# Performance work log

Measured on AMD Instinct MI355X. Metric: run time of the kernel, lower is better.

The kernel has to match this reference:

```python
import jax, jax.numpy as jnp
import numpy as np

T, N, F_IN, DZ = 4, 2048, 128, 128
HF = 256   # FEM output dim
H = 256    # EDM hidden dim
E1, E2 = 256, 64  # EAM dims


def _l2norm(x, axis):
    n = jnp.sqrt(jnp.sum(x * x, axis=axis, keepdims=True))
    return x / jnp.maximum(n, 1e-12)


def setup_inputs() -> dict:
    key = jax.random.key(0)
    ks = jax.random.split(key, 20)

    def lin(k, fi, fo):
        return (jax.random.normal(k, (fi, fo), jnp.float32) / np.float32(np.sqrt(fi)))

    sup = jax.random.uniform(ks[0], (T, N, N), jnp.float32)
    sup = sup / jnp.sum(sup, axis=2, keepdims=True)       # row-normalized GNN supports
    align = jax.random.uniform(ks[1], (T, N, N), jnp.float32)
    align = align / jnp.sum(align, axis=2, keepdims=True)  # row-normalized align matrices
    feat = jax.random.normal(ks[2], (T + 1, N, F_IN), jnp.float32)
    noise = jax.random.normal(ks[3], (T, N, DZ), jnp.float32)
    G_IN = HF + DZ   # 384
    EIN = H + HF     # 512
    return {
        "sup": sup, "feat": feat, "noise": noise, "align": align,
        "lambd": jnp.float32(0.4),
        "W_fem": lin(ks[4], F_IN, HF), "b_fem": jnp.zeros((HF,), jnp.float32),
        "W_gnn": lin(ks[5], G_IN, H), "b_gnn": jnp.zeros((H,), jnp.float32),
        "Wg_x": lin(ks[6], H, 2 * H), "Wg_h": lin(ks[7], H, 2 * H), "bg": jnp.zeros((2 * H,), jnp.float32),
        "Wc_x": lin(ks[8], H, H), "Wc_h": lin(ks[9], H, H), "bc": jnp.zeros((H,), jnp.float32),
        "W_att": lin(ks[10], HF, H), "b_att": jnp.zeros((H,), jnp.float32),
        "W_emb1": lin(ks[11], EIN, E1), "b_emb1": jnp.zeros((E1,), jnp.float32),
        "W_emb2": lin(ks[12], E1, E2), "b_emb2": jnp.zeros((E2,), jnp.float32),
        "W_scal1": lin(ks[13], EIN, E1), "b_scal1": jnp.zeros((E1,), jnp.float32),
        "W_scal2": lin(ks[14], E1, E2), "b_scal2": jnp.zeros((E2,), jnp.float32),
    }


def reference(sup, feat, noise, align, lambd,
              W_fem, b_fem, W_gnn, b_gnn,
              Wg_x, Wg_h, bg, Wc_x, Wc_h, bc,
              W_att, b_att,
              W_emb1, b_emb1, W_emb2, b_emb2,
              W_scal1, b_scal1, W_scal2, b_scal2):
    # --- FEM: shared linear + relu over all T+1 snapshots ---
    fem = jax.nn.relu(jnp.einsum('tnf,fh->tnh', feat, W_fem) + b_fem)  # [T+1,N,HF]
    t_win = sup.shape[0]
    edm_in = jnp.concatenate([fem[:t_win], noise], axis=2)             # [T,N,HF+DZ]

    # --- GNN (no time recurrence -> batched over T): relu((sup@x)W), row L2-norm ---
    agg = jnp.einsum('tnm,tmf->tnf', sup, edm_in)
    g = _l2norm(jax.nn.relu(jnp.einsum('tnf,fh->tnh', agg, W_gnn) + b_gnn), axis=2)

    # attention feature maps for the attentive node-aligning unit
    fm = jnp.einsum('tnf,fh->tnh', fem, W_att) + b_att                 # [T+1,N,H]
    h0 = jnp.zeros((sup.shape[1], W_gnn.shape[1]), dtype=feat.dtype)

    def step(h, x):
        gt, al, fsrc, fdst = x
        # IGRU cell
        gates = jax.nn.sigmoid(gt @ Wg_x + h @ Wg_h + bg)
        r, u = jnp.split(gates, 2, axis=1)
        c = jnp.tanh(gt @ Wc_x + (r * h) @ Wc_h + bc)
        rnn = (1.0 - u) * h + u * c
        # attentive node aligning: mix given align matrix with feature attention
        att = jax.nn.softmax(fdst @ fsrc.T, axis=1)                    # [N,N]
        sup_al = lambd * al + (1.0 - lambd) * att
        h_new = sup_al @ rnn
        return h_new, None

    h_last, _ = jax.lax.scan(step, h0, (g, align, fm[:t_win], fm[1:]))

    # --- EAM (pred_flag=True): tanh embedding head + sigmoid scaling head ---
    emb_cat = jnp.concatenate([h_last, fem[t_win]], axis=1)            # [N, H+HF]
    emb = jnp.tanh(jnp.tanh(emb_cat @ W_emb1 + b_emb1) @ W_emb2 + b_emb2)
    emb = _l2norm(emb, axis=0)                                         # F.normalize(dim=0)
    scal_o = jax.nn.sigmoid(jax.nn.sigmoid(emb_cat @ W_scal1 + b_scal1) @ W_scal2 + b_scal2)
    scal = scal_o @ scal_o.T                                           # [N,N]
    # pairwise-distance decoder: adj[i,j] = 1 + tanh(-||e_i - e_j||^2 * scal[i,j])
    sq = jnp.sum(emb * emb, axis=1)
    dist = -(sq[:, None] + sq[None, :] - 2.0 * (emb @ emb.T))
    return 1.0 + jnp.tanh(dist * scal)
```

## Files before the change

kernel.cpp:

```cpp
#include <hip/hip_runtime.h>
#include <math.h>


#define T_WIN 4
#define NN 2048
#define F_IN 128
#define HF 256
#define HH 256
#define DZ 128
#define G_IN 384
#define EIN 512
#define E1D 256
#define E2D 64

typedef _Float16 f16;
typedef _Float16 f16x8 __attribute__((ext_vector_type(8)));
typedef _Float16 f16x4 __attribute__((ext_vector_type(4)));
typedef float f32x4 __attribute__((ext_vector_type(4)));

__device__ __forceinline__ float wave_sum(float v) {
#pragma unroll
  for (int o = 32; o > 0; o >>= 1) v += __shfl_down(v, o);
  return v;
}
__device__ __forceinline__ float wave_max(float v) {
#pragma unroll
  for (int o = 32; o > 0; o >>= 1) v = fmaxf(v, __shfl_down(v, o));
  return v;
}

__device__ __forceinline__ void gld_lds16(const void* g, void* l) {
  __builtin_amdgcn_global_load_lds(
      (const __attribute__((address_space(1))) unsigned int*)g,
      (__attribute__((address_space(3))) unsigned int*)l, 16, 0, 0);
}

template <int EPI, int BN, int WOUT>
__global__ __launch_bounds__(256) void hgemm(
    const f16* __restrict__ A, const f16* __restrict__ A2,
    const f16* __restrict__ BT, const float* __restrict__ bias,
    const float* __restrict__ bias2, float* __restrict__ Cf,
    f16* __restrict__ Ch, int lda, int lda2, int kspl, int ldb,
    int ldc, int K, long zA, long zB, long zC) {
  constexpr int WN = BN / 2;
  constexpr int FN = WN / 16;
  constexpr int BI = BN / 32;
  __shared__ alignas(16) f16 As[128 * 64];
  __shared__ alignas(16) f16 Bs[BN * 64];
  const int tid = threadIdx.x;
  const int lane = tid & 63, wid = tid >> 6;
  const int wm = wid >> 1, wn = wid & 1;
  const int row0 = blockIdx.y * 128, col0 = blockIdx.x * BN;
  const long zb = blockIdx.z;
  A += zb * zA;
  BT += zb * zB;
  const int l8 = lane >> 3;
  const int lx = ((lane & 7) ^ l8) * 8;
  const int sw = (lane & 7) * 8;

  f32x4 acc[4][FN];
#pragma unroll
  for (int m = 0; m < 4; ++m)
#pragma unroll
    for (int n = 0; n < FN; ++n) acc[m][n] = (f32x4){0.f, 0.f, 0.f, 0.f};

  for (int k0 = 0; k0 < K; k0 += 64) {
#pragma unroll
    for (int i = 0; i < 4; ++i) {
      int r = wid * 32 + i * 8;
      const f16* src =
          (k0 < kspl) ? A + (size_t)(row0 + r + l8) * lda + k0 + lx
                      : A2 + (size_t)(row0 + r + l8) * lda2 + (k0 - kspl) + lx;
      gld_lds16(src, &As[r * 64]);
    }
#pragma unroll
    for (int i = 0; i < BI; ++i) {
      int r = wid * (BN / 4) + i * 8;
      gld_lds16(BT + (size_t)(col0 + r + l8) * ldb + k0 + lx, &Bs[r * 64]);
    }
    __syncthreads();
#pragma unroll
    for (int ks = 0; ks < 2; ++ks) {
      f16x8 af[4], bf[FN];
#pragma unroll
      for (int m = 0; m < 4; ++m)
        af[m] = *(const f16x8*)&As[((wm * 64 + m * 16 + (lane & 15)) * 64 +
                                    ks * 32 + (lane >> 4) * 8) ^ sw];
#pragma unroll
      for (int n = 0; n < FN; ++n)
        bf[n] = *(const f16x8*)&Bs[((wn * WN + n * 16 + (lane & 15)) * 64 +
                                    ks * 32 + (lane >> 4) * 8) ^ sw];
#pragma unroll
      for (int m = 0; m < 4; ++m)
#pragma unroll
        for (int n = 0; n < FN; ++n)
          acc[m][n] = __builtin_amdgcn_mfma_f32_16x16x32_f16(af[m], bf[n],
                                                             acc[m][n], 0, 0, 0);
    }
    __syncthreads();
  }

  const int cl = lane & 15, rh4 = (lane >> 4) * 4;
  float* Cfb = Cf + zb * zC;
  f16* Chb = Ch + zb * zC;
  const float* bp = (EPI == 5 && zb == 1) ? bias2 : bias;
#pragma unroll
  for (int m = 0; m < 4; ++m) {
#pragma unroll
    for (int n = 0; n < FN; ++n) {
      int cc = col0 + wn * WN + n * 16 + cl;
      float bv = 0.f;
      if (EPI == 6)
        bv = (cc < 256) ? bias[cc] : bias2[cc - 256];
      else if (bp)
        bv = bp[cc];
#pragma unroll
      for (int q = 0; q < 4; ++q) {
        size_t r = row0 + wm * 64 + m * 16 + rh4 + q;
        float v = acc[m][n][q] + bv;
        if (EPI == 1) v = fmaxf(v, 0.f);
        if (EPI == 5) v = (zb == 0) ? tanhf(v) : 1.f / (1.f + __expf(-v));
        if (EPI == 6) v = (cc < 256) ? tanhf(v) : 1.f / (1.f + __expf(-v));
        if (WOUT == 0 || WOUT == 2) Cfb[r * ldc + cc] = v;
        if (WOUT == 1 || WOUT == 2) Chb[r * ldc + cc] = (f16)v;
      }
    }
  }
}

__global__ __launch_bounds__(256) void sup_agg(
    const float* __restrict__ sup, const f16* __restrict__ edmT,
    f16* __restrict__ aggP) {
  __shared__ alignas(16) f16 As[64 * 64];
  __shared__ alignas(16) f16 Bs[192 * 64];
  const int tid = threadIdx.x;
  const int lane = tid & 63, wid = tid >> 6;
  const int m0 = blockIdx.x * 64, n0 = blockIdx.y * 192;
  const int t = blockIdx.z >> 2, kh = blockIdx.z & 3;
  const int l8 = lane >> 3;
  const int lx = ((lane & 7) ^ l8) * 8;
  const int sw = (lane & 7) * 8;
  const int cl = lane & 15, hi = lane >> 4;
  const int wm = wid >> 1, wn = wid & 1;
  const float* supT = sup + (size_t)t * NN * NN;
  const f16* edmTt = edmT + (size_t)t * G_IN * NN;

  f32x4 acc[2][6];
#pragma unroll
  for (int m = 0; m < 2; ++m)
#pragma unroll
    for (int n = 0; n < 6; ++n) acc[m][n] = (f32x4){0.f, 0.f, 0.f, 0.f};

  const int ar = tid >> 2;
  const int g0 = (tid & 3) * 2;
  const int kbeg = kh * 512;

  for (int k0 = kbeg; k0 < kbeg + 512; k0 += 64) {
    const float* ap = supT + (size_t)(m0 + ar) * NN + k0 + (tid & 3) * 16;
    float4 f0 = *(const float4*)ap;
    float4 f1 = *(const float4*)(ap + 4);
    float4 f2 = *(const float4*)(ap + 8);
    float4 f3 = *(const float4*)(ap + 12);
    f16x8 hv0 = {(f16)f0.x, (f16)f0.y, (f16)f0.z, (f16)f0.w,
                 (f16)f1.x, (f16)f1.y, (f16)f1.z, (f16)f1.w};
    f16x8 hv1 = {(f16)f2.x, (f16)f2.y, (f16)f2.z, (f16)f2.w,
                 (f16)f3.x, (f16)f3.y, (f16)f3.z, (f16)f3.w};
    *(f16x8*)&As[ar * 64 + ((g0 ^ (ar & 7)) * 8)] = hv0;
    *(f16x8*)&As[ar * 64 + (((g0 + 1) ^ (ar & 7)) * 8)] = hv1;
#pragma unroll
    for (int i = 0; i < 6; ++i) {
      int rn = wid * 48 + i * 8;
      gld_lds16(edmTt + (size_t)(n0 + rn + l8) * NN + k0 + lx, &Bs[rn * 64]);
    }
    __syncthreads();
#pragma unroll
    for (int ks = 0; ks < 2; ++ks) {
      f16x8 af[2], bf[6];
#pragma unroll
      for (int m = 0; m < 2; ++m)
        af[m] = *(const f16x8*)&As[((wm * 32 + m * 16 + cl) * 64 + ks * 32 +
                                    hi * 8) ^ sw];
#pragma unroll
      for (int n = 0; n < 6; ++n)
        bf[n] = *(const f16x8*)&Bs[((wn * 96 + n * 16 + cl) * 64 + ks * 32 +
                                    hi * 8) ^ sw];
#pragma unroll
      for (int m = 0; m < 2; ++m)
#pragma unroll
        for (int n = 0; n < 6; ++n)
          acc[m][n] = __builtin_amdgcn_mfma_f32_16x16x32_f16(af[m], bf[n],
                                                             acc[m][n], 0, 0, 0);
    }
    __syncthreads();
  }

  f16* dst = aggP + (size_t)kh * (4L * NN * G_IN) +
             ((size_t)t * NN + m0) * G_IN + n0;
#pragma unroll
  for (int m = 0; m < 2; ++m)
#pragma unroll
    for (int n = 0; n < 6; ++n)
#pragma unroll
      for (int q = 0; q < 4; ++q)
        dst[(size_t)(wm * 32 + m * 16 + hi * 4 + q) * G_IN + wn * 96 +
            n * 16 + cl] = (f16)acc[m][n][q];
}

__global__ __launch_bounds__(256) void gnn_l2(
    const f16* __restrict__ aggP, const f16* __restrict__ WgnnT,
    const float* __restrict__ bgnn, f16* __restrict__ g16) {
  __shared__ alignas(16) f16 As[32 * 64];
  __shared__ alignas(16) f16 Bs[256 * 64];
  __shared__ float red[4][32];
  const int tid = threadIdx.x;
  const int lane = tid & 63, wid = tid >> 6;
  const int m0 = blockIdx.x * 32;
  const int l8 = lane >> 3;
  const int lx = ((lane & 7) ^ l8) * 8;
  const int sw = (lane & 7) * 8;
  const int cl = lane & 15, hi = lane >> 4;
  const long PS = 4L * NN * G_IN;

  f32x4 acc[2][4];
#pragma unroll
  for (int m = 0; m < 2; ++m)
#pragma unroll
    for (int n = 0; n < 4; ++n) acc[m][n] = (f32x4){0.f, 0.f, 0.f, 0.f};

  const int ar = tid >> 3;
  const int acw = ((tid & 7) ^ (ar & 7)) * 8;

  for (int k0 = 0; k0 < G_IN; k0 += 64) {
    size_t gi = (size_t)(m0 + ar) * G_IN + k0 + ((tid & 7) * 8);
    f16x8 a0 = *(const f16x8*)(aggP + gi);
    f16x8 a1 = *(const f16x8*)(aggP + PS + gi);
    f16x8 a2 = *(const f16x8*)(aggP + 2 * PS + gi);
    f16x8 a3 = *(const f16x8*)(aggP + 3 * PS + gi);
    f16x8 s;
#pragma unroll
    for (int e = 0; e < 8; ++e)
      s[e] = (f16)((float)a0[e] + (float)a1[e] + (float)a2[e] + (float)a3[e]);
    *(f16x8*)&As[ar * 64 + acw] = s;
#pragma unroll
    for (int i = 0; i < 8; ++i) {
      int rn = wid * 64 + i * 8;
      gld_lds16(WgnnT + (size_t)(rn + l8) * G_IN + k0 + lx, &Bs[rn * 64]);
    }
    __syncthreads();
#pragma unroll
    for (int ks = 0; ks < 2; ++ks) {
      f16x8 af[2], bf[4];
#pragma unroll
      for (int m = 0; m < 2; ++m)
        af[m] = *(const f16x8*)&As[((m * 16 + cl) * 64 + ks * 32 + hi * 8) ^ sw];
#pragma unroll
      for (int n = 0; n < 4; ++n)
        bf[n] = *(const f16x8*)&Bs[((wid * 64 + n * 16 + cl) * 64 + ks * 32 +
                                    hi * 8) ^ sw];
#pragma unroll
      for (int m = 0; m < 2; ++m)
#pragma unroll
        for (int n = 0; n < 4; ++n)
          acc[m][n] = __builtin_amdgcn_mfma_f32_16x16x32_f16(af[m], bf[n],
                                                             acc[m][n], 0, 0, 0);
    }
    __syncthreads();
  }

#pragma unroll
  for (int m = 0; m < 2; ++m)
#pragma unroll
    for (int n = 0; n < 4; ++n) {
      float bv = bgnn[wid * 64 + n * 16 + cl];
#pragma unroll
      for (int q = 0; q < 4; ++q)
        acc[m][n][q] = fmaxf(acc[m][n][q] + bv, 0.f);
    }
#pragma unroll
  for (int m = 0; m < 2; ++m)
#pragma unroll
    for (int q = 0; q < 4; ++q) {
      float ss = 0.f;
#pragma unroll
      for (int n = 0; n < 4; ++n) ss += acc[m][n][q] * acc[m][n][q];
#pragma unroll
      for (int msk = 1; msk < 16; msk <<= 1) ss += __shfl_xor(ss, msk);
      if (cl == 0) red[wid][m * 16 + hi * 4 + q] = ss;
    }
  __syncthreads();
#pragma unroll
  for (int m = 0; m < 2; ++m)
#pragma unroll
    for (int q = 0; q < 4; ++q) {
      int row = m * 16 + hi * 4 + q;
      float tot = red[0][row] + red[1][row] + red[2][row] + red[3][row];
      float inv = 1.f / fmaxf(sqrtf(tot), 1e-12f);
#pragma unroll
      for (int n = 0; n < 4; ++n)
        g16[(size_t)(m0 + row) * 256 + wid * 64 + n * 16 + cl] =
            (f16)(acc[m][n][q] * inv);
    }
}

__global__ __launch_bounds__(256) void hsum4(const float* __restrict__ hP,
                                             float* __restrict__ hf,
                                             f16* __restrict__ h16) {
  long i = ((long)blockIdx.x * 256 + threadIdx.x) * 4;
  float4 a = *(const float4*)(hP + i);
  float4 b = *(const float4*)(hP + 524288 + i);
  float4 c = *(const float4*)(hP + 1048576 + i);
  float4 d = *(const float4*)(hP + 1572864 + i);
  float4 s = {a.x + b.x + c.x + d.x, a.y + b.y + c.y + d.y,
              a.z + b.z + c.z + d.z, a.w + b.w + c.w + d.w};
  *(float4*)(hf + i) = s;
  f16x4 o = {(f16)s.x, (f16)s.y, (f16)s.z, (f16)s.w};
  *(f16x4*)(h16 + i) = o;
}

__global__ __launch_bounds__(256) void rnn0_t(const f16* __restrict__ Xgc,
                                              const float* __restrict__ bg,
                                              const float* __restrict__ bc,
                                              f16* __restrict__ rnnT) {
  __shared__ float tile[32][33];
  int n0 = blockIdx.x * 32, k0 = blockIdx.y * 32;
  int tx = threadIdx.x & 31, ty = threadIdx.x >> 5;
#pragma unroll
  for (int i = 0; i < 32; i += 8) {
    int n = n0 + ty + i, k = k0 + tx;
    float u = 1.f / (1.f + __expf(-((float)Xgc[(size_t)n * 768 + 256 + k] +
                                    bg[256 + k])));
    float c = tanhf((float)Xgc[(size_t)n * 768 + 512 + k] + bc[k]);
    tile[ty + i][tx] = u * c;
  }
  __syncthreads();
#pragma unroll
  for (int i = 0; i < 32; i += 8)
    rnnT[(size_t)(k0 + ty + i) * NN + n0 + tx] = (f16)tile[tx][ty + i];
}

__global__ __launch_bounds__(256) void gru_step(
    const float* __restrict__ hP, const f16* __restrict__ Xgc,
    const f16* __restrict__ WghT, const f16* __restrict__ WchT,
    const float* __restrict__ bg, const float* __restrict__ bc,
    f16* __restrict__ rnnT) {
  __shared__ alignas(16) f16 A_s[16 * 264];
  __shared__ alignas(16) f16 rh_s[16 * 264];
  __shared__ float u_s[16 * 260];
  __shared__ float hf_s[16 * 260];
  __shared__ alignas(16) f16 tileT[256 * 24];
  const int tid = threadIdx.x;
  const int lane = tid & 63, wid = tid >> 6;
  const int cl = lane & 15, hi = lane >> 4;
  const int r0 = blockIdx.x * 16;

#pragma unroll
  for (int i = 0; i < 4; ++i) {
    int e = i * 256 + tid;
    int row = e >> 6, off = (e & 63) * 4;
    size_t gi = (size_t)(r0 + row) * 256 + off;
    float4 a = *(const float4*)(hP + gi);
    float4 b = *(const float4*)(hP + 524288 + gi);
    float4 c = *(const float4*)(hP + 1048576 + gi);
    float4 d = *(const float4*)(hP + 1572864 + gi);
    float4 s = {a.x + b.x + c.x + d.x, a.y + b.y + c.y + d.y,
                a.z + b.z + c.z + d.z, a.w + b.w + c.w + d.w};
    *(float4*)&hf_s[row * 260 + off] = s;
    f16x4 h4 = {(f16)s.x, (f16)s.y, (f16)s.z, (f16)s.w};
    *(f16x4*)&A_s[row * 264 + off] = h4;
  }
  __syncthreads();

  const int wc0 = wid * 128;
  f32x4 acc[8];
#pragma unroll
  for (int n = 0; n < 8; ++n) acc[n] = (f32x4){0.f, 0.f, 0.f, 0.f};
#pragma unroll
  for (int kk = 0; kk < 256; kk += 32) {
    f16x8 af = *(const f16x8*)&A_s[cl * 264 + kk + hi * 8];
#pragma unroll
    for (int n = 0; n < 8; ++n) {
      f16x8 bf = *(const f16x8*)(WghT + (size_t)(wc0 + n * 16 + cl) * 256 +
                                 kk + hi * 8);
      acc[n] = __builtin_amdgcn_mfma_f32_16x16x32_f16(af, bf, acc[n], 0, 0, 0);
    }
  }
#pragma unroll
  for (int n = 0; n < 8; ++n) {
    int cc = wc0 + n * 16 + cl;
    float bgv = bg[cc];
#pragma unroll
    for (int q = 0; q < 4; ++q) {
      int rl = hi * 4 + q;
      float v = acc[n][q] + bgv + (float)Xgc[(size_t)(r0 + rl) * 768 + cc];
      float sv = 1.f / (1.f + __expf(-v));
      if (cc < 256)
        rh_s[rl * 264 + cc] = (f16)(sv * hf_s[rl * 260 + cc]);
      else
        u_s[rl * 260 + cc - 256] = sv;
    }
  }
  __syncthreads();

  const int wc2 = wid * 64;
  f32x4 acc2[4];
#pragma unroll
  for (int n = 0; n < 4; ++n) acc2[n] = (f32x4){0.f, 0.f, 0.f, 0.f};
#pragma unroll
  for (int kk = 0; kk < 256; kk += 32) {
    f16x8 af = *(const f16x8*)&rh_s[cl * 264 + kk + hi * 8];
#pragma unroll
    for (int n = 0; n < 4; ++n) {
      f16x8 bf = *(const f16x8*)(WchT + (size_t)(wc2 + n * 16 + cl) * 256 +
                                 kk + hi * 8);
      acc2[n] = __builtin_amdgcn_mfma_f32_16x16x32_f16(af, bf, acc2[n], 0, 0, 0);
    }
  }
#pragma unroll
  for (int n = 0; n < 4; ++n) {
    int cc = wc2 + n * 16 + cl;
    float bcv = bc[cc];
#pragma unroll
    for (int q = 0; q < 4; ++q) {
      int rl = hi * 4 + q;
      float cv = tanhf(acc2[n][q] + bcv +
                       (float)Xgc[(size_t)(r0 + rl) * 768 + 512 + cc]);
      float u = u_s[rl * 260 + cc];
      float hv = hf_s[rl * 260 + cc];
      tileT[cc * 24 + rl] = (f16)((1.f - u) * hv + u * cv);
    }
  }
  __syncthreads();

  {
    int cc = tid;
    *(f16x8*)&rnnT[(size_t)cc * NN + r0] = *(const f16x8*)&tileT[cc * 24];
    *(f16x8*)&rnnT[(size_t)cc * NN + r0 + 8] =
        *(const f16x8*)&tileT[cc * 24 + 8];
  }
}

__global__ __launch_bounds__(256) void pq_decode(
    const f16* __restrict__ emb, const f16* __restrict__ scal,
    const float* __restrict__ sq, float* __restrict__ out) {
  __shared__ alignas(16) f16 EA[128 * 64], EB[128 * 64], SA[128 * 64],
      SB[128 * 64];
  const int tid = threadIdx.x;
  const int lane = tid & 63, wid = tid >> 6;
  const int wm = wid >> 1, wn = wid & 1;
  const int row0 = blockIdx.y * 128, col0 = blockIdx.x * 128;
  const int l8 = lane >> 3;
  const int lx = ((lane & 7) ^ l8) * 8;
  const int sw = (lane & 7) * 8;
#pragma unroll
  for (int i = 0; i < 2; ++i) {
    int r = wid * 16 + i * 8;
    gld_lds16(emb + (size_t)(row0 + r + l8) * 64 + lx, &EA[r * 64]);
    gld_lds16(emb + (size_t)(col0 + r + l8) * 64 + lx, &EB[r * 64]);
    gld_lds16(scal + (size_t)(row0 + r + l8) * 64 + lx, &SA[r * 64]);
    gld_lds16(scal + (size_t)(col0 + r + l8) * 64 + lx, &SB[r * 64]);
    int r2 = r + 64;
    gld_lds16(emb + (size_t)(row0 + r2 + l8) * 64 + lx, &EA[r2 * 64]);
    gld_lds16(emb + (size_t)(col0 + r2 + l8) * 64 + lx, &EB[r2 * 64]);
    gld_lds16(scal + (size_t)(row0 + r2 + l8) * 64 + lx, &SA[r2 * 64]);
    gld_lds16(scal + (size_t)(col0 + r2 + l8) * 64 + lx, &SB[r2 * 64]);
  }
  __syncthreads();
  f32x4 accP[4][4], accQ[4][4];
#pragma unroll
  for (int m = 0; m < 4; ++m)
#pragma unroll
    for (int n = 0; n < 4; ++n) {
      accP[m][n] = (f32x4){0.f, 0.f, 0.f, 0.f};
      accQ[m][n] = (f32x4){0.f, 0.f, 0.f, 0.f};
    }
#pragma unroll
  for (int ks = 0; ks < 2; ++ks) {
    f16x8 af[4], bf[4];
#pragma unroll
    for (int m = 0; m < 4; ++m)
      af[m] = *(const f16x8*)&EA[((wm * 64 + m * 16 + (lane & 15)) * 64 +
                                  ks * 32 + (lane >> 4) * 8) ^ sw];
#pragma unroll
    for (int n = 0; n < 4; ++n)
      bf[n] = *(const f16x8*)&EB[((wn * 64 + n * 16 + (lane & 15)) * 64 +
                                  ks * 32 + (lane >> 4) * 8) ^ sw];
#pragma unroll
    for (int m = 0; m < 4; ++m)
#pragma unroll
      for (int n = 0; n < 4; ++n)
        accP[m][n] = __builtin_amdgcn_mfma_f32_16x16x32_f16(af[m], bf[n],
                                                            accP[m][n], 0, 0, 0);
#pragma unroll
    for (int m = 0; m < 4; ++m)
      af[m] = *(const f16x8*)&SA[((wm * 64 + m * 16 + (lane & 15)) * 64 +
                                  ks * 32 + (lane >> 4) * 8) ^ sw];
#pragma unroll
    for (int n = 0; n < 4; ++n)
      bf[n] = *(const f16x8*)&SB[((wn * 64 + n * 16 + (lane & 15)) * 64 +
                                  ks * 32 + (lane >> 4) * 8) ^ sw];
#pragma unroll
    for (int m = 0; m < 4; ++m)
#pragma unroll
      for (int n = 0; n < 4; ++n)
        accQ[m][n] = __builtin_amdgcn_mfma_f32_16x16x32_f16(af[m], bf[n],
                                                            accQ[m][n], 0, 0, 0);
  }
  const int cl = lane & 15, rh4 = (lane >> 4) * 4;
#pragma unroll
  for (int m = 0; m < 4; ++m) {
#pragma unroll
    for (int n = 0; n < 4; ++n) {
      int c = col0 + wn * 64 + n * 16 + cl;
      float sqc = sq[c];
#pragma unroll
      for (int q = 0; q < 4; ++q) {
        size_t r = row0 + wm * 64 + m * 16 + rh4 + q;
        float dist = -(sq[r] + sqc - 2.f * accP[m][n][q]);
        out[r * NN + c] = 1.f + tanhf(dist * accQ[m][n][q]);
      }
    }
  }
}

struct MT {
  const float* src[11];
  f16* dst[11];
  int K[11], N[11], st[11], ts[12];
};
__global__ __launch_bounds__(256) void multi_transp(MT mt) {
  __shared__ float tile[32][33];
  int b = blockIdx.x, w = 0;
  while (b >= mt.ts[w + 1]) ++w;
  int lt = b - mt.ts[w];
  int K = mt.K[w], N = mt.N[w];
  int tk = lt % (K >> 5), tn = lt / (K >> 5);
  int k0 = tk * 32, n0 = tn * 32;
  int tx = threadIdx.x & 31, ty = threadIdx.x >> 5;
  const float* src = mt.src[w];
#pragma unroll
  for (int i = 0; i < 32; i += 8)
    tile[ty + i][tx] = src[(size_t)(k0 + ty + i) * N + n0 + tx];
  __syncthreads();
  f16* dst = mt.dst[w];
  int st = mt.st[w];
#pragma unroll
  for (int i = 0; i < 32; i += 8)
    dst[(size_t)(n0 + ty + i) * st + k0 + tx] = (f16)tile[tx][ty + i];
}

__global__ __launch_bounds__(256) void edm_t(const f16* __restrict__ fem16,
                                             const float* __restrict__ noise,
                                             f16* __restrict__ edmT) {
  __shared__ float tile[32][33];
  int bx = blockIdx.x, r0 = blockIdx.y * 32, t = blockIdx.z;
  int tx = threadIdx.x & 31, ty = threadIdx.x >> 5;
  f16* dstT = edmT + (size_t)t * G_IN * NN;
  if (bx < 8) {
    int c0 = bx * 32;
    const f16* src = fem16 + (size_t)t * NN * HF;
#pragma unroll
    for (int i = 0; i < 32; i += 8)
      tile[ty + i][tx] = (float)src[(size_t)(r0 + ty + i) * HF + c0 + tx];
    __syncthreads();
#pragma unroll
    for (int i = 0; i < 32; i += 8)
      dstT[(size_t)(c0 + ty + i) * NN + r0 + tx] = (f16)tile[tx][ty + i];
  } else {
    int c0 = (bx - 8) * 32;
    const float* src = noise + (size_t)t * NN * DZ;
#pragma unroll
    for (int i = 0; i < 32; i += 8)
      tile[ty + i][tx] = src[(size_t)(r0 + ty + i) * DZ + c0 + tx];
    __syncthreads();
#pragma unroll
    for (int i = 0; i < 32; i += 8)
      dstT[(size_t)(HF + c0 + ty + i) * NN + r0 + tx] = (f16)tile[tx][ty + i];
  }
}

__global__ __launch_bounds__(256) void cvt_h(const float* __restrict__ in,
                                             f16* __restrict__ out) {
  long i = ((long)blockIdx.x * 256 + threadIdx.x) * 4;
  float4 v = *(const float4*)(in + i);
  f16x4 o = {(f16)v.x, (f16)v.y, (f16)v.z, (f16)v.w};
  *(f16x4*)(out + i) = o;
}

__global__ __launch_bounds__(256) void softmax_mix(
    const float* __restrict__ S, const float* __restrict__ Al,
    const float* __restrict__ lam_ptr, f16* __restrict__ Mh) {
  const int tid = threadIdx.x;
  const float4* s4 = (const float4*)(S + (long)blockIdx.x * 2048);
  float4 a = s4[tid], b = s4[tid + 256];
  float m = fmaxf(fmaxf(fmaxf(a.x, a.y), fmaxf(a.z, a.w)),
                  fmaxf(fmaxf(b.x, b.y), fmaxf(b.z, b.w)));
  __shared__ float red[4];
  float w = wave_max(m);
  if ((tid & 63) == 0) red[tid >> 6] = w;
  __syncthreads();
  m = fmaxf(fmaxf(red[0], red[1]), fmaxf(red[2], red[3]));
  __syncthreads();
  a.x = __expf(a.x - m); a.y = __expf(a.y - m);
  a.z = __expf(a.z - m); a.w = __expf(a.w - m);
  b.x = __expf(b.x - m); b.y = __expf(b.y - m);
  b.z = __expf(b.z - m); b.w = __expf(b.w - m);
  float s = a.x + a.y + a.z + a.w + b.x + b.y + b.z + b.w;
  w = wave_sum(s);
  if ((tid & 63) == 0) red[tid >> 6] = w;
  __syncthreads();
  float inv = 1.f / (red[0] + red[1] + red[2] + red[3]);
  float lam = lam_ptr[0], oml = 1.f - lam;
  const float4* al4 = (const float4*)(Al + (long)blockIdx.x * 2048);
  float4 x = al4[tid], y = al4[tid + 256];
  f16x4 o0 = {(f16)(lam * x.x + oml * a.x * inv),
              (f16)(lam * x.y + oml * a.y * inv),
              (f16)(lam * x.z + oml * a.z * inv),
              (f16)(lam * x.w + oml * a.w * inv)};
  f16x4 o1 = {(f16)(lam * y.x + oml * b.x * inv),
              (f16)(lam * y.y + oml * b.y * inv),
              (f16)(lam * y.z + oml * b.z * inv),
              (f16)(lam * y.w + oml * b.w * inv)};
  f16x4* out4 = (f16x4*)(Mh + (long)blockIdx.x * 2048);
  out4[tid] = o0;
  out4[tid + 256] = o1;
}

__global__ __launch_bounds__(256) void col_l2norm64(
    const float* __restrict__ x, float* __restrict__ cn) {
  int c = blockIdx.x;
  float ss = 0.f;
  for (int r = threadIdx.x; r < NN; r += 256) {
    float v = x[(long)r * 64 + c];
    ss += v * v;
  }
  __shared__ float red[4];
  float w = wave_sum(ss);
  if ((threadIdx.x & 63) == 0) red[threadIdx.x >> 6] = w;
  __syncthreads();
  if (threadIdx.x == 0)
    cn[c] = fmaxf(sqrtf(red[0] + red[1] + red[2] + red[3]), 1e-12f);
}

__global__ void norm_sq64h(const float* __restrict__ x,
                           const float* __restrict__ cn,
                           f16* __restrict__ emb16, float* __restrict__ sq) {
  int i = blockIdx.x, j = threadIdx.x;
  float e = x[(long)i * 64 + j] / cn[j];
  emb16[(long)i * 64 + j] = (f16)e;
  float s = wave_sum(e * e);
  if (j == 0) sq[i] = s;
}

extern "C" void kernel_launch(void* const* d_in, const int* in_sizes, int n_in,
                              void* d_out, int out_size, void* d_ws,
                              size_t ws_size, hipStream_t stream) {
  (void)in_sizes; (void)n_in; (void)out_size; (void)ws_size;
  const float* sup    = (const float*)d_in[0];
  const float* feat   = (const float*)d_in[1];
  const float* noise  = (const float*)d_in[2];
  const float* align  = (const float*)d_in[3];
  const float* lambd  = (const float*)d_in[4];
  const float* W_fem  = (const float*)d_in[5];
  const float* b_fem  = (const float*)d_in[6];
  const float* W_gnn  = (const float*)d_in[7];
  const float* b_gnn  = (const float*)d_in[8];
  const float* Wg_x   = (const float*)d_in[9];
  const float* Wg_h   = (const float*)d_in[10];
  const float* bg     = (const float*)d_in[11];
  const float* Wc_x   = (const float*)d_in[12];
  const float* Wc_h   = (const float*)d_in[13];
  const float* bc     = (const float*)d_in[14];
  const float* W_att  = (const float*)d_in[15];
  const float* b_att  = (const float*)d_in[16];
  const float* W_emb1 = (const float*)d_in[17];
  const float* b_emb1 = (const float*)d_in[18];
  const float* W_emb2 = (const float*)d_in[19];
  const float* b_emb2 = (const float*)d_in[20];
  const float* W_scal1= (const float*)d_in[21];
  const float* b_scal1= (const float*)d_in[22];
  const float* W_scal2= (const float*)d_in[23];
  const float* b_scal2= (const float*)d_in[24];

  char* wsb = (char*)d_ws;
  size_t po = 0;
  auto P = [&](size_t bytes) {
    size_t r = po;
    po += (bytes + 255) & ~(size_t)255;
    return r;
  };
  f16* fem16  = (f16*)(wsb + P(5L * NN * HF * 2));
  f16* fm16   = (f16*)(wsb + P(5L * NN * HH * 2));
  f16* g16    = (f16*)(wsb + P(4L * NN * HH * 2));
  f16* WT     = (f16*)(wsb + P(884736L * 2));
  f16* Xgc16  = (f16*)(wsb + P(4L * NN * 768 * 2));
  float* hA   = (float*)(wsb + P((long)NN * HH * 4));
  f16* h16A   = (f16*)(wsb + P((long)NN * HH * 2));
  f16* rnnT16 = (f16*)(wsb + P((long)NN * HH * 2));
  float* hP   = (float*)(wsb + P(4L * NN * HH * 4));
  f16* M16_2  = (f16*)(wsb + P(2L * NN * NN * 2));
  f16* e1s1   = (f16*)(wsb + P((long)NN * 512 * 2));
  float* embscF = (float*)(wsb + P(2L * NN * E2D * 4));
  f16* embsc16  = (f16*)(wsb + P(2L * NN * E2D * 2));
  f16* emb16  = (f16*)(wsb + P((long)NN * E2D * 2));
  float* cn   = (float*)(wsb + P(64 * 4));
  float* sq   = (float*)(wsb + P(NN * 4));
  size_t arena = P(34078720);
  f16* feat16 = (f16*)(wsb + arena);
  f16* edmT   = (f16*)(wsb + arena + 2621440);
  f16* aggP   = (f16*)(wsb + arena + 8912896);
  float* Sbuf2 = (float*)(wsb + arena);

  f16* W_femT  = WT;
  f16* W_gnnT  = W_femT + 32768;
  f16* WgxcT   = W_gnnT + 98304;
  f16* WghT    = WgxcT + 196608;
  f16* WchT    = WghT + 131072;
  f16* W_attT  = WchT + 65536;
  f16* We1s1T  = W_attT + 65536;
  f16* Wemb2T  = We1s1T + 262144;
  f16* Wscal2T = Wemb2T + 16384;

  MT mt;
  const float* wsrc[11] = {W_fem, W_gnn, Wg_x, Wc_x, Wg_h, Wc_h,
                           W_att, W_emb1, W_scal1, W_emb2, W_scal2};
  f16* wdst[11] = {W_femT, W_gnnT, WgxcT, WgxcT + 512 * 256, WghT, WchT,
                   W_attT, We1s1T, We1s1T + 256 * 512, Wemb2T, Wscal2T};
  const int wK[11]  = {128, 384, 256, 256, 256, 256, 256, 512, 512, 256, 256};
  const int wNd[11] = {256, 256, 512, 256, 512, 256, 256, 256, 256, 64, 64};
  const int wSt[11] = {128, 384, 256, 256, 256, 256, 256, 512, 512, 256, 256};
  int tcum = 0;
  for (int i = 0; i < 11; ++i) {
    mt.src[i] = wsrc[i];
    mt.dst[i] = wdst[i];
    mt.K[i] = wK[i];
    mt.N[i] = wNd[i];
    mt.st[i] = wSt[i];
    mt.ts[i] = tcum;
    tcum += (wK[i] >> 5) * (wNd[i] >> 5);
  }
  mt.ts[11] = tcum;

  const f16* NH = nullptr;
  float* NF = nullptr;
  f16* NHm = nullptr;

  multi_transp<<<tcum, 256, 0, stream>>>(mt);
  cvt_h<<<(5L * NN * F_IN) / 1024, 256, 0, stream>>>(feat, feat16);

  hgemm<1, 64, 1><<<dim3(4, 80, 1), 256, 0, stream>>>(
      feat16, NH, W_femT, b_fem, nullptr, NF, fem16,
      128, 0, 128, 128, 256, 128, 0, 0, 0);

  edm_t<<<dim3(12, 64, 4), 256, 0, stream>>>(fem16, noise, edmT);

  sup_agg<<<dim3(32, 2, 16), 256, 0, stream>>>(sup, edmT, aggP);
  gnn_l2<<<256, 256, 0, stream>>>(aggP, W_gnnT, b_gnn, g16);

  hgemm<0, 64, 1><<<dim3(4, 80, 1), 256, 0, stream>>>(
      fem16, NH, W_attT, b_att, nullptr, NF, fm16,
      256, 0, 256, 256, 256, 256, 0, 0, 0);

  hgemm<0, 64, 1><<<dim3(12, 64, 1), 256, 0, stream>>>(
      g16, NH, WgxcT, nullptr, nullptr, NF, Xgc16,
      256, 0, 256, 256, 768, 256, 0, 0, 0);

  for (int p = 0; p < 2; ++p) {
    hgemm<0, 128, 0><<<dim3(16, 16, 2), 256, 0, stream>>>(
        fm16 + (size_t)(2 * p + 1) * NN * HH, NH,
        fm16 + (size_t)(2 * p) * NN * HH, nullptr, nullptr, Sbuf2, NHm,
        256, 0, 256, 256, 2048, 256, (long)NN * HH, (long)NN * HH,
        (long)NN * NN);
    softmax_mix<<<2 * NN, 256, 0, stream>>>(
        Sbuf2, align + (size_t)(2 * p) * NN * NN, lambd, M16_2);

    for (int tl = 0; tl < 2; ++tl) {
      int t = 2 * p + tl;
      if (t == 0) {
        rnn0_t<<<dim3(64, 8, 1), 256, 0, stream>>>(Xgc16, bg, bc, rnnT16);
      } else {
        gru_step<<<128, 256, 0, stream>>>(
            hP, Xgc16 + (size_t)t * NN * 768, WghT, WchT, bg, bc, rnnT16);
      }
      hgemm<0, 64, 0><<<dim3(4, 16, 4), 256, 0, stream>>>(
          M16_2 + (size_t)(t & 1) * NN * NN, NH, rnnT16, nullptr, nullptr,
          hP, NHm, 2048, 0, 2048, 2048, 256, 512, 512, 512, 524288);
    }
  }
  hsum4<<<512, 256, 0, stream>>>(hP, hA, h16A);

  hgemm<6, 64, 1><<<dim3(8, 16, 1), 256, 0, stream>>>(
      h16A, fem16 + 4L * NN * HF, We1s1T, b_emb1, b_scal1, NF, e1s1,
      256, 256, 256, 512, 512, 512, 0, 0, 0);
  hgemm<5, 64, 2><<<dim3(1, 16, 2), 256, 0, stream>>>(
      e1s1, NH, Wemb2T, b_emb2, b_scal2, embscF, embsc16,
      512, 0, 512, 256, 64, 256, 256, 16384, (long)NN * E2D);
  col_l2norm64<<<64, 256, 0, stream>>>(embscF, cn);
  norm_sq64h<<<NN, 64, 0, stream>>>(embscF, cn, emb16, sq);

  pq_decode<<<dim3(16, 16, 1), 256, 0, stream>>>(
      emb16, embsc16 + (size_t)NN * E2D, sq, (float*)d_out);
}
```

Baseline: 317.0 us.

## Reassociate GNN layer to apply W_gnn before support aggregation

Measured after the change: 315.5 us. No clear change (-0.5%).

```diff
diff --git a/kernel.cpp b/kernel.cpp
--- a/kernel.cpp
+++ b/kernel.cpp
@@ -40,8 +40,8 @@
     const f16* __restrict__ A, const f16* __restrict__ A2,
     const f16* __restrict__ BT, const float* __restrict__ bias,
     const float* __restrict__ bias2, float* __restrict__ Cf,
-    f16* __restrict__ Ch, int lda, int lda2, int kspl, int ldb,
-    int ldc, int K, long zA, long zB, long zC) {
+    f16* __restrict__ Ch, int lda, int lda2, int kspl, int ldb, int ldc,
+    int K, long zA, long zA2, long zB, long zC) {
   constexpr int WN = BN / 2;
   constexpr int FN = WN / 16;
   constexpr int BI = BN / 32;
@@ -53,6 +53,7 @@
   const int row0 = blockIdx.y * 128, col0 = blockIdx.x * BN;
   const long zb = blockIdx.z;
   A += zb * zA;
+  if (A2) A2 += zb * zA2;
   BT += zb * zB;
   const int l8 = lane >> 3;
   const int lx = ((lane & 7) ^ l8) * 8;
@@ -128,14 +129,14 @@
   }
 }
 
-__global__ __launch_bounds__(256) void sup_agg(
-    const float* __restrict__ sup, const f16* __restrict__ edmT,
+__global__ __launch_bounds__(256) void sup_gnn2(
+    const float* __restrict__ sup, const f16* __restrict__ edmWT,
     f16* __restrict__ aggP) {
   __shared__ alignas(16) f16 As[64 * 64];
-  __shared__ alignas(16) f16 Bs[192 * 64];
+  __shared__ alignas(16) f16 Bs[128 * 64];
   const int tid = threadIdx.x;
   const int lane = tid & 63, wid = tid >> 6;
-  const int m0 = blockIdx.x * 64, n0 = blockIdx.y * 192;
+  const int m0 = blockIdx.x * 64, n0 = blockIdx.y * 128;
   const int t = blockIdx.z >> 2, kh = blockIdx.z & 3;
   const int l8 = lane >> 3;
   const int lx = ((lane & 7) ^ l8) * 8;
@@ -143,13 +144,13 @@
   const int cl = lane & 15, hi = lane >> 4;
   const int wm = wid >> 1, wn = wid & 1;
   const float* supT = sup + (size_t)t * NN * NN;
-  const f16* edmTt = edmT + (size_t)t * G_IN * NN;
-
-  f32x4 acc[2][6];
+  const f16* BTt = edmWT + (size_t)t * 256 * NN;
+
+  f32x4 acc[2][4];
 #pragma unroll
   for (int m = 0; m < 2; ++m)
 #pragma unroll
-    for (int n = 0; n < 6; ++n) acc[m][n] = (f32x4){0.f, 0.f, 0.f, 0.f};
+    for (int n = 0; n < 4; ++n) acc[m][n] = (f32x4){0.f, 0.f, 0.f, 0.f};
 
   const int ar = tid >> 2;
   const int g0 = (tid & 3) * 2;
@@ -168,94 +169,21 @@
     *(f16x8*)&As[ar * 64 + ((g0 ^ (ar & 7)) * 8)] = hv0;
     *(f16x8*)&As[ar * 64 + (((g0 + 1) ^ (ar & 7)) * 8)] = hv1;
 #pragma unroll
-    for (int i = 0; i < 6; ++i) {
-      int rn = wid * 48 + i * 8;
-      gld_lds16(edmTt + (size_t)(n0 + rn + l8) * NN + k0 + lx, &Bs[rn * 64]);
+    for (int i = 0; i < 4; ++i) {
+      int rn = wid * 32 + i * 8;
+      gld_lds16(BTt + (size_t)(n0 + rn + l8) * NN + k0 + lx, &Bs[rn * 64]);
     }
     __syncthreads();
 #pragma unroll
     for (int ks = 0; ks < 2; ++ks) {
-      f16x8 af[2], bf[6];
+      f16x8 af[2], bf[4];
 #pragma unroll
       for (int m = 0; m < 2; ++m)
         af[m] = *(const f16x8*)&As[((wm * 32 + m * 16 + cl) * 64 + ks * 32 +
                                     hi * 8) ^ sw];
 #pragma unroll
-      for (int n = 0; n < 6; ++n)
-        bf[n] = *(const f16x8*)&Bs[((wn * 96 + n * 16 + cl) * 64 + ks * 32 +
-                                    hi * 8) ^ sw];
-#pragma unroll
-      for (int m = 0; m < 2; ++m)
-#pragma unroll
-        for (int n = 0; n < 6; ++n)
-          acc[m][n] = __builtin_amdgcn_mfma_f32_16x16x32_f16(af[m], bf[n],
-                                                             acc[m][n], 0, 0, 0);
-    }
-    __syncthreads();
-  }
-
-  f16* dst = aggP + (size_t)kh * (4L * NN * G_IN) +
-             ((size_t)t * NN + m0) * G_IN + n0;
-#pragma unroll
-  for (int m = 0; m < 2; ++m)
-#pragma unroll
-    for (int n = 0; n < 6; ++n)
-#pragma unroll
-      for (int q = 0; q < 4; ++q)
-        dst[(size_t)(wm * 32 + m * 16 + hi * 4 + q) * G_IN + wn * 96 +
-            n * 16 + cl] = (f16)acc[m][n][q];
-}
-
-__global__ __launch_bounds__(256) void gnn_l2(
-    const f16* __restrict__ aggP, const f16* __restrict__ WgnnT,
-    const float* __restrict__ bgnn, f16* __restrict__ g16) {
-  __shared__ alignas(16) f16 As[32 * 64];
-  __shared__ alignas(16) f16 Bs[256 * 64];
-  __shared__ float red[4][32];
-  const int tid = threadIdx.x;
-  const int lane = tid & 63, wid = tid >> 6;
-  const int m0 = blockIdx.x * 32;
-  const int l8 = lane >> 3;
-  const int lx = ((lane & 7) ^ l8) * 8;
-  const int sw = (lane & 7) * 8;
-  const int cl = lane & 15, hi = lane >> 4;
-  const long PS = 4L * NN * G_IN;
-
-  f32x4 acc[2][4];
-#pragma unroll
-  for (int m = 0; m < 2; ++m)
-#pragma unroll
-    for (int n = 0; n < 4; ++n) acc[m][n] = (f32x4){0.f, 0.f, 0.f, 0.f};
-
-  const int ar = tid >> 3;
-  const int acw = ((tid & 7) ^ (ar & 7)) * 8;
-
-  for (int k0 = 0; k0 < G_IN; k0 += 64) {
-    size_t gi = (size_t)(m0 + ar) * G_IN + k0 + ((tid & 7) * 8);
-    f16x8 a0 = *(const f16x8*)(aggP + gi);
-    f16x8 a1 = *(const f16x8*)(aggP + PS + gi);
-    f16x8 a2 = *(const f16x8*)(aggP + 2 * PS + gi);
-    f16x8 a3 = *(const f16x8*)(aggP + 3 * PS + gi);
-    f16x8 s;
-#pragma unroll
-    for (int e = 0; e < 8; ++e)
-      s[e] = (f16)((float)a0[e] + (float)a1[e] + (float)a2[e] + (float)a3[e]);
-    *(f16x8*)&As[ar * 64 + acw] = s;
-#pragma unroll
-    for (int i = 0; i < 8; ++i) {
-      int rn = wid * 64 + i * 8;
-      gld_lds16(WgnnT + (size_t)(rn + l8) * G_IN + k0 + lx, &Bs[rn * 64]);
-    }
-    __syncthreads();
-#pragma unroll
-    for (int ks = 0; ks < 2; ++ks) {
-      f16x8 af[2], bf[4];
-#pragma unroll
-      for (int m = 0; m < 2; ++m)
-        af[m] = *(const f16x8*)&As[((m * 16 + cl) * 64 + ks * 32 + hi * 8) ^ sw];
-#pragma unroll
       for (int n = 0; n < 4; ++n)
-        bf[n] = *(const f16x8*)&Bs[((wid * 64 + n * 16 + cl) * 64 + ks * 32 +
+        bf[n] = *(const f16x8*)&Bs[((wn * 64 + n * 16 + cl) * 64 + ks * 32 +
                                     hi * 8) ^ sw];
 #pragma unroll
       for (int m = 0; m < 2; ++m)
@@ -267,39 +195,62 @@
     __syncthreads();
   }
 
+  f16* dst = aggP + (size_t)kh * (4L * NN * 256) +
+             ((size_t)t * NN + m0) * 256 + n0;
 #pragma unroll
   for (int m = 0; m < 2; ++m)
 #pragma unroll
-    for (int n = 0; n < 4; ++n) {
-      float bv = bgnn[wid * 64 + n * 16 + cl];
+    for (int n = 0; n < 4; ++n)
 #pragma unroll
       for (int q = 0; q < 4; ++q)
-        acc[m][n][q] = fmaxf(acc[m][n][q] + bv, 0.f);
-    }
-#pragma unroll
-  for (int m = 0; m < 2; ++m)
-#pragma unroll
-    for (int q = 0; q < 4; ++q) {
-      float ss = 0.f;
-#pragma unroll
-      for (int n = 0; n < 4; ++n) ss += acc[m][n][q] * acc[m][n][q];
-#pragma unroll
-      for (int msk = 1; msk < 16; msk <<= 1) ss += __shfl_xor(ss, msk);
-      if (cl == 0) red[wid][m * 16 + hi * 4 + q] = ss;
-    }
-  __syncthreads();
-#pragma unroll
-  for (int m = 0; m < 2; ++m)
-#pragma unroll
-    for (int q = 0; q < 4; ++q) {
-      int row = m * 16 + hi * 4 + q;
-      float tot = red[0][row] + red[1][row] + red[2][row] + red[3][row];
-      float inv = 1.f / fmaxf(sqrtf(tot), 1e-12f);
-#pragma unroll
-      for (int n = 0; n < 4; ++n)
-        g16[(size_t)(m0 + row) * 256 + wid * 64 + n * 16 + cl] =
-            (f16)(acc[m][n][q] * inv);
-    }
+        dst[(size_t)(wm * 32 + m * 16 + hi * 4 + q) * 256 + wn * 64 +
+            n * 16 + cl] = (f16)acc[m][n][q];
+}
+
+__global__ __launch_bounds__(256) void gnn_fin(const f16* __restrict__ aggP,
+                                               const float* __restrict__ bgnn,
+                                               f16* __restrict__ g16) {
+  const int tid = threadIdx.x;
+  const int lane = tid & 63, w = tid >> 6;
+  const size_t r = (size_t)blockIdx.x * 4 + w;
+  const long PS = 4L * NN * 256;
+  size_t gi = r * 256 + lane * 4;
+  f16x4 a0 = *(const f16x4*)(aggP + gi);
+  f16x4 a1 = *(const f16x4*)(aggP + PS + gi);
+  f16x4 a2 = *(const f16x4*)(aggP + 2 * PS + gi);
+  f16x4 a3 = *(const f16x4*)(aggP + 3 * PS + gi);
+  float v[4];
+  float ss = 0.f;
+#pragma unroll
+  for (int j = 0; j < 4; ++j) {
+    v[j] = (float)a0[j] + (float)a1[j] + (float)a2[j] + (float)a3[j] +
+           bgnn[lane * 4 + j];
+    v[j] = fmaxf(v[j], 0.f);
+    ss += v[j] * v[j];
+  }
+  float tot = wave_sum(ss);
+  tot = __shfl(tot, 0);
+  float inv = 1.f / fmaxf(sqrtf(tot), 1e-12f);
+  f16x4 o = {(f16)(v[0] * inv), (f16)(v[1] * inv), (f16)(v[2] * inv),
+             (f16)(v[3] * inv)};
+  *(f16x4*)(g16 + gi) = o;
+}
+
+__global__ __launch_bounds__(256) void transp_h(const f16* __restrict__ in,
+                                                f16* __restrict__ out, int R,
+                                                int C, long sIn, long sOut) {
+  in += blockIdx.z * sIn;
+  out += blockIdx.z * sOut;
+  __shared__ float tile[32][33];
+  int c0 = blockIdx.x * 32, r0 = blockIdx.y * 32;
+  int tx = threadIdx.x & 31, ty = threadIdx.x >> 5;
+#pragma unroll
+  for (int i = 0; i < 32; i += 8)
+    tile[ty + i][tx] = (float)in[(size_t)(r0 + ty + i) * C + c0 + tx];
+  __syncthreads();
+#pragma unroll
+  for (int i = 0; i < 32; i += 8)
+    out[(size_t)(c0 + ty + i) * R + r0 + tx] = (f16)tile[tx][ty + i];
 }
 
 __global__ __launch_bounds__(256) void hsum4(const float* __restrict__ hP,
@@ -430,7 +381,6 @@
     }
   }
   __syncthreads();
-
   {
     int cc = tid;
     *(f16x8*)&rnnT[(size_t)cc * NN + r0] = *(const f16x8*)&tileT[cc * 24];
@@ -548,49 +498,30 @@
     dst[(size_t)(n0 + ty + i) * st + k0 + tx] = (f16)tile[tx][ty + i];
 }
 
-__global__ __launch_bounds__(256) void edm_t(const f16* __restrict__ fem16,
-                                             const float* __restrict__ noise,
-                                             f16* __restrict__ edmT) {
-  __shared__ float tile[32][33];
-  int bx = blockIdx.x, r0 = blockIdx.y * 32, t = blockIdx.z;
-  int tx = threadIdx.x & 31, ty = threadIdx.x >> 5;
-  f16* dstT = edmT + (size_t)t * G_IN * NN;
-  if (bx < 8) {
-    int c0 = bx * 32;
-    const f16* src = fem16 + (size_t)t * NN * HF;
-#pragma unroll
-    for (int i = 0; i < 32; i += 8)
-      tile[ty + i][tx] = (float)src[(size_t)(r0 + ty + i) * HF + c0 + tx];
-    __syncthreads();
-#pragma unroll
-    for (int i = 0; i < 32; i += 8)
-      dstT[(size_t)(c0 + ty + i) * NN + r0 + tx] = (f16)tile[tx][ty + i];
+__global__ __launch_bounds__(256) void cvt2(const float* __restrict__ feat,
+                                            f16* __restrict__ feat16,
+                                            const float* __restrict__ noise,
+                                            f16* __restrict__ noise16) {
+  const long FN4 = 5L * NN * F_IN;
+  long i = ((long)blockIdx.x * 256 + threadIdx.x) * 4;
+  const float* src;
+  f16* dst;
+  long j;
+  if (i < FN4) {
+    src = feat; dst = feat16; j = i;
   } else {
-    int c0 = (bx - 8) * 32;
-    const float* src = noise + (size_t)t * NN * DZ;
-#pragma unroll
-    for (int i = 0; i < 32; i += 8)
-      tile[ty + i][tx] = src[(size_t)(r0 + ty + i) * DZ + c0 + tx];
-    __syncthreads();
-#pragma unroll
-    for (int i = 0; i < 32; i += 8)
-      dstT[(size_t)(HF + c0 + ty + i) * NN + r0 + tx] = (f16)tile[tx][ty + i];
-  }
-}
-
-__global__ __launch_bounds__(256) void cvt_h(const float* __restrict__ in,
-                                             f16* __restrict__ out) {
-  long i = ((long)blockIdx.x * 256 + threadIdx.x) * 4;
-  float4 v = *(const float4*)(in + i);
+    src = noise; dst = noise16; j = i - FN4;
+  }
+  float4 v = *(const float4*)(src + j);
   f16x4 o = {(f16)v.x, (f16)v.y, (f16)v.z, (f16)v.w};
-  *(f16x4*)(out + i) = o;
+  *(f16x4*)(dst + j) = o;
 }
 
 __global__ __launch_bounds__(256) void softmax_mix(
     const float* __restrict__ S, const float* __restrict__ Al,
     const float* __restrict__ lam_ptr, f16* __restrict__ Mh) {
   const int tid = threadIdx.x;
-  const float4* s4 = (const float4*)(S + (long)blockIdx.x * 2048);
+  const float4* s4 = (const float4*)(S + (size_t)blockIdx.x * 2048);
   float4 a = s4[tid], b = s4[tid + 256];
   float m = fmaxf(fmaxf(fmaxf(a.x, a.y), fmaxf(a.z, a.w)),
                   fmaxf(fmaxf(b.x, b.y), fmaxf(b.z, b.w)));
@@ -610,7 +541,7 @@
   __syncthreads();
   float inv = 1.f / (red[0] + red[1] + red[2] + red[3]);
   float lam = lam_ptr[0], oml = 1.f - lam;
-  const float4* al4 = (const float4*)(Al + (long)blockIdx.x * 2048);
+  const float4* al4 = (const float4*)(Al + (size_t)blockIdx.x * 2048);
   float4 x = al4[tid], y = al4[tid + 256];
   f16x4 o0 = {(f16)(lam * x.x + oml * a.x * inv),
               (f16)(lam * x.y + oml * a.y * inv),
@@ -620,7 +551,7 @@
               (f16)(lam * y.y + oml * b.y * inv),
               (f16)(lam * y.z + oml * b.z * inv),
               (f16)(lam * y.w + oml * b.w * inv)};
-  f16x4* out4 = (f16x4*)(Mh + (long)blockIdx.x * 2048);
+  f16x4* out4 = (f16x4*)(Mh + (size_t)blockIdx.x * 2048);
   out4[tid] = o0;
   out4[tid + 256] = o1;
 }
@@ -705,9 +636,11 @@
   float* cn   = (float*)(wsb + P(64 * 4));
   float* sq   = (float*)(wsb + P(NN * 4));
   size_t arena = P(34078720);
-  f16* feat16 = (f16*)(wsb + arena);
-  f16* edmT   = (f16*)(wsb + arena + 2621440);
-  f16* aggP   = (f16*)(wsb + arena + 8912896);
+  f16* feat16  = (f16*)(wsb + arena);
+  f16* noise16 = (f16*)(wsb + arena + 2621440);
+  f16* edmW    = (f16*)(wsb + arena + 4718592);
+  f16* edmWT   = (f16*)(wsb + arena + 8912896);
+  f16* aggP    = (f16*)(wsb + arena + 13107200);
   float* Sbuf2 = (float*)(wsb + arena);
 
   f16* W_femT  = WT;
@@ -745,31 +678,38 @@
   f16* NHm = nullptr;
 
   multi_transp<<<tcum, 256, 0, stream>>>(mt);
-  cvt_h<<<(5L * NN * F_IN) / 1024, 256, 0, stream>>>(feat, feat16);
+  cvt2<<<(5L * NN * F_IN + 4L * NN * DZ) / 1024, 256, 0, stream>>>(
+      feat, feat16, noise, noise16);
 
   hgemm<1, 64, 1><<<dim3(4, 80, 1), 256, 0, stream>>>(
       feat16, NH, W_femT, b_fem, nullptr, NF, fem16,
-      128, 0, 128, 128, 256, 128, 0, 0, 0);
-
-  edm_t<<<dim3(12, 64, 4), 256, 0, stream>>>(fem16, noise, edmT);
-
-  sup_agg<<<dim3(32, 2, 16), 256, 0, stream>>>(sup, edmT, aggP);
-  gnn_l2<<<256, 256, 0, stream>>>(aggP, W_gnnT, b_gnn, g16);
+      128, 0, 128, 128, 256, 128, 0, 0, 0, 0);
+
+  hgemm<0, 64, 1><<<dim3(4, 16, 4), 256, 0, stream>>>(
+      fem16, noise16, W_gnnT, nullptr, nullptr, NF, edmW,
+      256, 128, 256, 384, 256, 384,
+      (long)NN * HF, (long)NN * DZ, 0, (long)NN * 256);
+
+  transp_h<<<dim3(8, 64, 4), 256, 0, stream>>>(
+      edmW, edmWT, NN, 256, (long)NN * 256, 256L * NN);
+
+  sup_gnn2<<<dim3(32, 2, 16), 256, 0, stream>>>(sup, edmWT, aggP);
+  gnn_fin<<<2048, 256, 0, stream>>>(aggP, b_gnn, g16);
 
   hgemm<0, 64, 1><<<dim3(4, 80, 1), 256, 0, stream>>>(
       fem16, NH, W_attT, b_att, nullptr, NF, fm16,
-      256, 0, 256, 256, 256, 256, 0, 0, 0);
+      256, 0, 256, 256, 256, 256, 0, 0, 0, 0);
 
   hgemm<0, 64, 1><<<dim3(12, 64, 1), 256, 0, stream>>>(
       g16, NH, WgxcT, nullptr, nullptr, NF, Xgc16,
-      256, 0, 256, 256, 768, 256, 0, 0, 0);
+      256, 0, 256, 256, 768, 256, 0, 0, 0, 0);
 
   for (int p = 0; p < 2; ++p) {
     hgemm<0, 128, 0><<<dim3(16, 16, 2), 256, 0, stream>>>(
         fm16 + (size_t)(2 * p + 1) * NN * HH, NH,
         fm16 + (size_t)(2 * p) * NN * HH, nullptr, nullptr, Sbuf2, NHm,
-        256, 0, 256, 256, 2048, 256, (long)NN * HH, (long)NN * HH,
-        (long)NN * NN);
+        256, 0, 256, 256, 2048, 256,
+        (long)NN * HH, 0, (long)NN * HH, (long)NN * NN);
     softmax_mix<<<2 * NN, 256, 0, stream>>>(
         Sbuf2, align + (size_t)(2 * p) * NN * NN, lambd, M16_2);
 
@@ -783,17 +723,18 @@
       }
       hgemm<0, 64, 0><<<dim3(4, 16, 4), 256, 0, stream>>>(
           M16_2 + (size_t)(t & 1) * NN * NN, NH, rnnT16, nullptr, nullptr,
-          hP, NHm, 2048, 0, 2048, 2048, 256, 512, 512, 512, 524288);
+          hP, NHm, 2048, 0, 2048, 2048, 256, 512,
+          512, 0, 512, 524288);
     }
   }
   hsum4<<<512, 256, 0, stream>>>(hP, hA, h16A);
 
   hgemm<6, 64, 1><<<dim3(8, 16, 1), 256, 0, stream>>>(
       h16A, fem16 + 4L * NN * HF, We1s1T, b_emb1, b_scal1, NF, e1s1,
-      256, 256, 256, 512, 512, 512, 0, 0, 0);
+      256, 256, 256, 512, 512, 512, 0, 0, 0, 0);
   hgemm<5, 64, 2><<<dim3(1, 16, 2), 256, 0, stream>>>(
       e1s1, NH, Wemb2T, b_emb2, b_scal2, embscF, embsc16,
-      512, 0, 512, 256, 64, 256, 256, 16384, (long)NN * E2D);
+      512, 0, 512, 256, 64, 256, 256, 0, 16384, (long)NN * E2D);
   col_l2norm64<<<64, 256, 0, stream>>>(embscF, cn);
   norm_sq64h<<<NN, 64, 0, stream>>>(embscF, cn, emb16, sq);
 
```
